# Performance work log

Hardware: AMD Instinct MI355X
Metric: run time of the kernel (lower is better)

## Reference

```python
import jax, jax.numpy as jnp
import numpy as np
from jax import lax

INPUT_SIZE = 64
HIDDEN_SIZE = 4096
OUTPUT_SIZE = 16
SEQ_LEN = 4096
SPECTRAL_RADIUS = 0.95
LEAKY_RATE = 0.9
INPUT_SCALING = 1.0
FEEDBACK_SCALING = 0.1
SPARSITY = 0.1


def setup_inputs() -> dict:
    key = jax.random.key(0)
    ks = jax.random.split(key, 7)
    X = jax.random.normal(ks[0], (SEQ_LEN, INPUT_SIZE), dtype=jnp.float32)
    W_in = jax.random.normal(ks[1], (HIDDEN_SIZE, INPUT_SIZE), dtype=jnp.float32) * INPUT_SCALING
    # sparse reservoir matrix, scaled so spectral radius ~ SPECTRAL_RADIUS
    dense = jax.random.normal(ks[2], (HIDDEN_SIZE, HIDDEN_SIZE), dtype=jnp.float32)
    mask = (jax.random.uniform(ks[3], (HIDDEN_SIZE, HIDDEN_SIZE)) < SPARSITY).astype(jnp.float32)
    # circular-law estimate of spectral radius for sparse gaussian: sqrt(density*N)
    scale = SPECTRAL_RADIUS / np.sqrt(SPARSITY * HIDDEN_SIZE)
    W_res = dense * mask * scale
    b = jax.random.normal(ks[4], (HIDDEN_SIZE,), dtype=jnp.float32)
    W_fb = jax.random.normal(ks[5], (HIDDEN_SIZE, OUTPUT_SIZE), dtype=jnp.float32) * FEEDBACK_SCALING
    W_out = jax.random.normal(ks[6], (OUTPUT_SIZE, HIDDEN_SIZE), dtype=jnp.float32) * 0.01
    return {"X": X, "W_in": W_in, "W_res": W_res, "b": b, "W_fb": W_fb, "W_out": W_out}


def reference(X, W_in, W_res, b, W_fb, W_out):
    """ESN with feedback + leaky integration; Force readout (inference: y = W_out @ s).
    Returns (results [T, O], outputs [T, H]) matching ESNForce.forward."""
    H = W_res.shape[0]
    O = W_out.shape[0]

    def step(carry, x_t):
        s, y = carry  # previous state [H], previous output [O]
        pre = W_in @ x_t + W_res @ s + b + W_fb @ y
        s_new = (1.0 - LEAKY_RATE) * s + LEAKY_RATE * jnp.tanh(pre)
        y_new = W_out @ s_new
        return (s_new, y_new), (y_new, s_new)

    init = (jnp.zeros((H,), dtype=X.dtype), jnp.zeros((O,), dtype=X.dtype))
    _, (results, outputs) = lax.scan(step, init, X)
    return results, outputs
```

## Files before the change

kernel.cpp:

```cpp
#include <hip/hip_runtime.h>
#include <cstdint>

#define NBLK 128
#define BLOCK 1024
#define ROWS 32
#define HDIM 4096
#define IDIM 64
#define ODIM 16
#define TSTEPS 4096
#define PAD 576
#define RNDS 9
#define LEAK 0.9f
#define FSTR 16

typedef float f32x4 __attribute__((ext_vector_type(4)));

__global__ void init_ws(unsigned* ws) {
    int i = blockIdx.x * blockDim.x + threadIdx.x;
    if (i < NBLK * FSTR)
        __hip_atomic_store(&ws[i], 0u, __ATOMIC_RELAXED, __HIP_MEMORY_SCOPE_AGENT);
}

__global__ __launch_bounds__(BLOCK) void esn_kernel(
    const float* __restrict__ X,
    const float* __restrict__ Win,
    const float* __restrict__ Wres,
    const float* __restrict__ bvec,
    const float* __restrict__ Wfb,
    const float* __restrict__ Wout,
    float* __restrict__ out,
    float* __restrict__ part,
    unsigned* __restrict__ flags)
{
    __shared__ float          ell_val[ROWS][PAD];
    __shared__ unsigned short ell_idx[ROWS][PAD];
    __shared__ __align__(16) float s_lds[HDIM];
    __shared__ float          win_lds[ROWS][IDIM];
    __shared__ float          wfb_lds[ROWS][ODIM];
    __shared__ __align__(16) float wout_lds[ROWS][ODIM];
    __shared__ float          b_lds[ROWS];
    __shared__ float          x_lds[IDIM];
    __shared__ float          y_lds[ODIM];
    __shared__ __align__(16) float snew_lds[ROWS];
    __shared__ unsigned       prog[NBLK];

    const int tid   = threadIdx.x;
    const int blk   = blockIdx.x;
    const int rbase = blk * ROWS;

    {
        const int wave = tid >> 6;
        const int lane = tid & 63;
        for (int rr = wave * 2; rr < wave * 2 + 2; ++rr) {
            const float* wrow = Wres + (size_t)(rbase + rr) * HDIM;
            int base = 0;
            for (int c0 = 0; c0 < HDIM; c0 += 64) {
                float w = wrow[c0 + lane];
                unsigned long long m = __ballot(w != 0.0f);
                int before = __popcll(m & ((1ull << lane) - 1ull));
                if (w != 0.0f && (base + before) < PAD) {
                    ell_val[rr][base + before] = w;
                    ell_idx[rr][base + before] = (unsigned short)(c0 + lane);
                }
                base += __popcll(m);
            }
            if (base > PAD) base = PAD;
            for (int e = base + lane; e < PAD; e += 64) {
                ell_val[rr][e] = 0.0f;
                ell_idx[rr][e] = 0;
            }
        }
    }
    for (int i = tid; i < ROWS * IDIM; i += BLOCK)
        win_lds[i >> 6][i & 63] = Win[(size_t)(rbase + (i >> 6)) * IDIM + (i & 63)];
    for (int i = tid; i < ROWS * ODIM; i += BLOCK)
        wfb_lds[i >> 4][i & 15] = Wfb[(size_t)(rbase + (i >> 4)) * ODIM + (i & 15)];
    for (int i = tid; i < ROWS * ODIM; i += BLOCK)
        wout_lds[i >> 4][i & 15] = Wout[(size_t)(i & 15) * HDIM + rbase + (i >> 4)];
    if (tid < ROWS) b_lds[tid] = bvec[rbase + tid];

    for (int i = tid; i < HDIM; i += BLOCK) s_lds[i] = 0.0f;
    if (tid < ODIM) y_lds[tid] = 0.0f;
    if (tid >= 64 && tid < 128) x_lds[tid - 64] = X[tid - 64];
    if (tid < NBLK) prog[tid] = 0u;
    __syncthreads();

    float* out_res = out;
    float* out_s   = out + (size_t)TSTEPS * ODIM;

    for (int t = 0; t < TSTEPS; ++t) {
        {
            const int row = tid >> 5;
            const int l   = tid & 31;
            float a0 = 0.0f, a1 = 0.0f;
            #pragma unroll
            for (int k = 0; k < RNDS; ++k) {
                const int e = (k << 6) + (l << 1);
                const float2  v  = *(const float2*)&ell_val[row][e];
                const ushort2 ix = *(const ushort2*)&ell_idx[row][e];
                a0 += v.x * s_lds[ix.x];
                a1 += v.y * s_lds[ix.y];
            }
            float acc = a0 + a1;
            acc += win_lds[row][l] * x_lds[l] + win_lds[row][l + 32] * x_lds[l + 32];
            if (l < ODIM) acc += wfb_lds[row][l] * y_lds[l];
            acc += __shfl_xor(acc, 16, 32);
            acc += __shfl_xor(acc, 8, 32);
            acc += __shfl_xor(acc, 4, 32);
            acc += __shfl_xor(acc, 2, 32);
            acc += __shfl_xor(acc, 1, 32);
            if (l == 0) {
                const float pre = acc + b_lds[row];
                snew_lds[row] = (1.0f - LEAK) * s_lds[rbase + row] + LEAK * tanhf(pre);
            }
        }
        __syncthreads();

        const int wv = tid >> 6;
        const int ln = tid & 63;
        if (wv == 0) {
            if (ln < ROWS / 4) {
                f32x4 v4 = *(const f32x4*)&snew_lds[ln * 4];
                float* dst = out_s + (size_t)t * HDIM + rbase + ln * 4;
                asm volatile("global_store_dwordx4 %0, %1, off sc0 sc1"
                             :: "v"(dst), "v"(v4) : "memory");
            }
            if (ln < ODIM / 4) {
                f32x4 acc = {0.0f, 0.0f, 0.0f, 0.0f};
                #pragma unroll
                for (int r = 0; r < ROWS; ++r) {
                    f32x4 w = *(const f32x4*)&wout_lds[r][ln * 4];
                    acc += w * snew_lds[r];
                }
                float* dst = part + ((size_t)(t & 1) * NBLK + blk) * ODIM + ln * 4;
                asm volatile("global_store_dwordx4 %0, %1, off sc0 sc1"
                             :: "v"(dst), "v"(acc) : "memory");
            }
            if (ln == 0)
                __hip_atomic_store(&flags[blk * FSTR], (unsigned)(t + 1),
                                   __ATOMIC_RELEASE, __HIP_MEMORY_SCOPE_AGENT);
        } else if (wv == 1) {
            if (t + 1 < TSTEPS) x_lds[ln] = X[(size_t)(t + 1) * IDIM + ln];
            const unsigned tu = (unsigned)(t + 1);
            for (;;) {
                unsigned f0 = __hip_atomic_load(&flags[ln * FSTR],        __ATOMIC_RELAXED, __HIP_MEMORY_SCOPE_AGENT);
                unsigned f1 = __hip_atomic_load(&flags[(ln + 64) * FSTR], __ATOMIC_RELAXED, __HIP_MEMORY_SCOPE_AGENT);
                __hip_atomic_store(&prog[ln],      f0, __ATOMIC_RELAXED, __HIP_MEMORY_SCOPE_WORKGROUP);
                __hip_atomic_store(&prog[ln + 64], f1, __ATOMIC_RELAXED, __HIP_MEMORY_SCOPE_WORKGROUP);
                if (__all(f0 >= tu && f1 >= tu)) break;
                __builtin_amdgcn_s_sleep(1);
            }
            asm volatile("" ::: "memory");
            const int o = ln & 15, j = ln >> 4;
            float* pb = part + (size_t)(t & 1) * NBLK * ODIM;
            float acc = 0.0f;
            #pragma unroll
            for (int k = 0; k < 32; ++k)
                acc += __hip_atomic_load(pb + (size_t)(j + 4 * k) * ODIM + o,
                                         __ATOMIC_RELAXED, __HIP_MEMORY_SCOPE_AGENT);
            acc += __shfl_xor(acc, 16);
            acc += __shfl_xor(acc, 32);
            if (ln < ODIM) {
                if (t + 1 < TSTEPS) y_lds[ln] = acc;
                if (blk == 0) out_res[(size_t)t * ODIM + ln] = acc;
            }
        } else {
            if (t + 1 < TSTEPS) {
                const int wi    = wv - 2;
                const int start = (wi < 2) ? wi * 10 : 20 + (wi - 2) * 9;
                const int count = (wi < 2) ? 10 : 9;
                const unsigned tu = (unsigned)(t + 1);
                for (;;) {
                    unsigned f = (ln < count)
                        ? __hip_atomic_load(&prog[start + ln], __ATOMIC_RELAXED, __HIP_MEMORY_SCOPE_WORKGROUP)
                        : tu;
                    if (__all(f >= tu)) break;
                    __builtin_amdgcn_s_sleep(1);
                }
                asm volatile("" ::: "memory");
                const int c0 = start * ROWS;
                const int n4 = count * (ROWS / 4);
                const float* base = out_s + (size_t)t * HDIM + c0;
                for (int i = ln; i < n4; i += 64) {
                    f32x4 v;
                    const float* p = base + i * 4;
                    asm volatile("global_load_dwordx4 %0, %1, off sc0 sc1"
                                 : "=v"(v) : "v"(p) : "memory");
                    asm volatile("s_waitcnt vmcnt(0)" ::: "memory");
                    *(f32x4*)&s_lds[c0 + i * 4] = v;
                }
            }
        }
        __syncthreads();
    }
}

extern "C" void kernel_launch(void* const* d_in, const int* in_sizes, int n_in,
                              void* d_out, int out_size, void* d_ws, size_t ws_size,
                              hipStream_t stream) {
    (void)in_sizes; (void)n_in; (void)out_size; (void)ws_size;
    const float* X    = (const float*)d_in[0];
    const float* Win  = (const float*)d_in[1];
    const float* Wres = (const float*)d_in[2];
    const float* b    = (const float*)d_in[3];
    const float* Wfb  = (const float*)d_in[4];
    const float* Wout = (const float*)d_in[5];
    float* out = (float*)d_out;
    unsigned* flags = (unsigned*)d_ws;
    float* part = (float*)d_ws + NBLK * FSTR;

    init_ws<<<8, 256, 0, stream>>>(flags);
    esn_kernel<<<NBLK, BLOCK, 0, stream>>>(X, Win, Wres, b, Wfb, Wout, out, part, flags);
}
```

Before: 22.65 ms.

## Bank-aware ELL packing with per-row round count and overlapped state reloads

Rebuilds the per-row sparse ELL layout so each row's nonzeros are spread into groups by column bank, which reduces LDS bank conflicts on the gathered s_lds reads. Each row now runs only as many rounds as its nonzero count requires, replacing the fixed unrolled count of 9. The state reload loop issues both global loads before a single waitcnt, so the two loads overlap. Setup becomes a serial single-lane pass over each row and the inner loop is no longer unrolled, so the compiler has less freedom to schedule it.

```diff
diff --git a/kernel.cpp b/kernel.cpp
--- a/kernel.cpp
+++ b/kernel.cpp
@@ -9,7 +9,7 @@
 #define ODIM 16
 #define TSTEPS 4096
 #define PAD 576
-#define RNDS 9
+#define GMAX 18
 #define LEAK 0.9f
 #define FSTR 16
 
@@ -43,34 +43,76 @@
     __shared__ float          y_lds[ODIM];
     __shared__ __align__(16) float snew_lds[ROWS];
     __shared__ unsigned       prog[NBLK];
+    __shared__ int            nnz_lds[ROWS];
+    __shared__ int            rnds_lds[ROWS];
+    __shared__ unsigned short bankCnt[ROWS][32];
+    __shared__ unsigned short grpCnt[ROWS][GMAX];
 
     const int tid   = threadIdx.x;
     const int blk   = blockIdx.x;
     const int rbase = blk * ROWS;
 
+    for (int i = tid; i < ROWS * PAD; i += BLOCK) {
+        ell_val[i / PAD][i % PAD] = 0.0f;
+        ell_idx[i / PAD][i % PAD] = 0;
+    }
+    for (int i = tid; i < ROWS * 32; i += BLOCK) bankCnt[i >> 5][i & 31] = 0;
+    for (int i = tid; i < ROWS * GMAX; i += BLOCK) grpCnt[i / GMAX][i % GMAX] = 0;
+
     {
-        const int wave = tid >> 6;
-        const int lane = tid & 63;
+        const int wave = tid >> 6, lane = tid & 63;
         for (int rr = wave * 2; rr < wave * 2 + 2; ++rr) {
             const float* wrow = Wres + (size_t)(rbase + rr) * HDIM;
-            int base = 0;
-            for (int c0 = 0; c0 < HDIM; c0 += 64) {
-                float w = wrow[c0 + lane];
-                unsigned long long m = __ballot(w != 0.0f);
-                int before = __popcll(m & ((1ull << lane) - 1ull));
-                if (w != 0.0f && (base + before) < PAD) {
-                    ell_val[rr][base + before] = w;
-                    ell_idx[rr][base + before] = (unsigned short)(c0 + lane);
+            int cnt = 0;
+            for (int c0 = 0; c0 < HDIM; c0 += 64)
+                cnt += __popcll(__ballot(wrow[c0 + lane] != 0.0f));
+            if (lane == 0) {
+                int nz = cnt < PAD ? cnt : PAD;
+                nnz_lds[rr] = nz;
+                int gu = (nz + 31) >> 5;
+                if (gu < 1) gu = 1;
+                if (gu > GMAX) gu = GMAX;
+                rnds_lds[rr] = (gu + 1) >> 1;
+            }
+        }
+    }
+    __syncthreads();
+
+    {
+        const int wave = tid >> 6, lane = tid & 63;
+        if (lane == 0 || lane == 32) {
+            const int row = wave * 2 + (lane >> 5);
+            const int nz  = nnz_lds[row];
+            int gu = (nz + 31) >> 5;
+            if (gu < 1) gu = 1;
+            if (gu > GMAX) gu = GMAX;
+            const float* wrow = Wres + (size_t)(rbase + row) * HDIM;
+            int placed = 0;
+            for (int c = 0; c < HDIM && placed < nz; ++c) {
+                const float w = wrow[c];
+                if (w != 0.0f) {
+                    const int b = c & 31;
+                    const int r = bankCnt[row][b];
+                    bankCnt[row][b] = (unsigned short)(r + 1);
+                    int g = r % gu;
+                    int p = grpCnt[row][g];
+                    int guard = 0;
+                    while (p >= 32 && guard < GMAX) {
+                        g = (g + 1 == gu) ? 0 : g + 1;
+                        p = grpCnt[row][g];
+                        ++guard;
+                    }
+                    if (p >= 32) break;
+                    grpCnt[row][g] = (unsigned short)(p + 1);
+                    const int slot = ((g >> 1) << 6) + 2 * p + (g & 1);
+                    ell_val[row][slot] = w;
+                    ell_idx[row][slot] = (unsigned short)c;
+                    ++placed;
                 }
-                base += __popcll(m);
-            }
-            if (base > PAD) base = PAD;
-            for (int e = base + lane; e < PAD; e += 64) {
-                ell_val[rr][e] = 0.0f;
-                ell_idx[rr][e] = 0;
-            }
-        }
-    }
+            }
+        }
+    }
+
     for (int i = tid; i < ROWS * IDIM; i += BLOCK)
         win_lds[i >> 6][i & 63] = Win[(size_t)(rbase + (i >> 6)) * IDIM + (i & 63)];
     for (int i = tid; i < ROWS * ODIM; i += BLOCK)
@@ -92,9 +134,9 @@
         {
             const int row = tid >> 5;
             const int l   = tid & 31;
+            const int R   = rnds_lds[row];
             float a0 = 0.0f, a1 = 0.0f;
-            #pragma unroll
-            for (int k = 0; k < RNDS; ++k) {
+            for (int k = 0; k < R; ++k) {
                 const int e = (k << 6) + (l << 1);
                 const float2  v  = *(const float2*)&ell_val[row][e];
                 const ushort2 ix = *(const ushort2*)&ell_idx[row][e];
@@ -181,14 +223,18 @@
                 const int c0 = start * ROWS;
                 const int n4 = count * (ROWS / 4);
                 const float* base = out_s + (size_t)t * HDIM + c0;
-                for (int i = ln; i < n4; i += 64) {
-                    f32x4 v;
-                    const float* p = base + i * 4;
+                f32x4 v0, v1;
+                const float* p0 = base + (size_t)ln * 4;
+                asm volatile("global_load_dwordx4 %0, %1, off sc0 sc1"
+                             : "=v"(v0) : "v"(p0));
+                const bool has2 = (ln + 64) < n4;
+                const float* p1 = base + (size_t)(ln + 64) * 4;
+                if (has2)
                     asm volatile("global_load_dwordx4 %0, %1, off sc0 sc1"
-                                 : "=v"(v) : "v"(p) : "memory");
-                    asm volatile("s_waitcnt vmcnt(0)" ::: "memory");
-                    *(f32x4*)&s_lds[c0 + i * 4] = v;
-                }
+                                 : "=v"(v1) : "v"(p1));
+                asm volatile("s_waitcnt vmcnt(0)" ::: "memory");
+                *(f32x4*)&s_lds[c0 + ln * 4] = v0;
+                if (has2) *(f32x4*)&s_lds[c0 + (ln + 64) * 4] = v1;
             }
         }
         __syncthreads();
```

Result: faster. 21.98 ms (-2.9%).
